# Kernel tuning notes

Measured on AMD Instinct MI355X. Metric: run time of the kernel, lower is better.

## Reference

```python
import jax, jax.numpy as jnp
import numpy as np

N = 4096      # tokens per modality
DIM = 514     # input feature dim
OUT = 256     # out_dim (per-head width, head=1)
NC = 2        # num_classes
LN_EPS = 1e-5


def setup_inputs() -> dict:
    key = jax.random.key(0)
    ks = jax.random.split(key, 12)
    def nrm(k, shape, s=0.02):
        return jax.random.normal(k, shape, dtype=jnp.float32) * s
    return {
        "t1": jax.random.normal(ks[0], (N, DIM), dtype=jnp.float32),
        "t2": jax.random.normal(ks[1], (N, DIM), dtype=jnp.float32),
        "t1c": jax.random.normal(ks[2], (N, DIM), dtype=jnp.float32),
        "Wqkv1": nrm(ks[3], (DIM, 3 * OUT)), "bqkv1": jnp.zeros((3 * OUT,), jnp.float32),
        "Wqkv2": nrm(ks[4], (DIM, 3 * OUT)), "bqkv2": jnp.zeros((3 * OUT,), jnp.float32),
        "Wqkv3": nrm(ks[5], (DIM, 3 * OUT)), "bqkv3": jnp.zeros((3 * OUT,), jnp.float32),
        "Wo1": nrm(ks[6], (2 * OUT, DIM)), "bo1": jnp.zeros((DIM,), jnp.float32),
        "Wo2": nrm(ks[7], (2 * OUT, DIM)), "bo2": jnp.zeros((DIM,), jnp.float32),
        "Wo3": nrm(ks[8], (2 * OUT, DIM)), "bo3": jnp.zeros((DIM,), jnp.float32),
        "ln_g": jnp.ones((3 * DIM,), jnp.float32),
        "ln_b": jnp.zeros((3 * DIM,), jnp.float32),
        "Wh": nrm(ks[9], (3 * DIM, NC)), "bh": jnp.zeros((NC,), jnp.float32),
    }


def _forward(t1, t2, t1c, Wqkv1, bqkv1, Wqkv2, bqkv2, Wqkv3, bqkv3,
             Wo1, bo1, Wo2, bo2, Wo3, bo3, ln_g, ln_b, Wh, bh):
    # QKV projections (head=1 so no head reshape needed)
    q1, k1, v1 = jnp.split(t1 @ Wqkv1 + bqkv1, 3, axis=-1)   # each [n, OUT]
    q2, k2, v2 = jnp.split(t2 @ Wqkv2 + bqkv2, 3, axis=-1)
    q3, k3, v3 = jnp.split(t1c @ Wqkv3 + bqkv3, 3, axis=-1)

    # Six cross-attention instances batched into one group dim g=6.
    # Order: out12, out13, out21, out23, out31, out32  (q_x attends to k_y/v_y)
    qs = jnp.stack([q2, q3, q1, q3, q1, q2])                  # [6, n, OUT]
    ks_ = jnp.stack([k1, k1, k2, k2, k3, k3])
    vs = jnp.stack([v1, v1, v2, v2, v3, v3])
    # NOTE: original code applies NO 1/sqrt(d) scale
    attn = jax.nn.softmax(jnp.einsum('gid,gjd->gij', qs, ks_), axis=-1)
    outs = jnp.einsum('gij,gjd->gid', attn, vs)               # [6, n, OUT]
    out12, out13, out21, out23, out31, out32 = outs

    # residual add with duplicated keys, then per-modality output proj + residual
    t1r = jnp.concatenate([out21, out31], -1) + jnp.concatenate([k1, k1], -1)
    t2r = jnp.concatenate([out12, out32], -1) + jnp.concatenate([k2, k2], -1)
    t3r = jnp.concatenate([out13, out23], -1) + jnp.concatenate([k3, k3], -1)
    a1 = t1r @ Wo1 + bo1 + t1                                 # [n, DIM]
    a2 = t2r @ Wo2 + bo2 + t2
    a3 = t3r @ Wo3 + bo3 + t1c

    atten = jnp.concatenate([a1, a2, a3], -1)                 # [n, 3*DIM]
    mu = jnp.mean(atten, axis=-1, keepdims=True)
    var = jnp.var(atten, axis=-1, keepdims=True)
    normed = (atten - mu) * jax.lax.rsqrt(var + LN_EPS) * ln_g + ln_b
    out = normed @ Wh + bh                                    # [n, NC]
    feat = atten[None]                                        # [1, n, 3*DIM]
    return out, feat


def reference(t1, t2, t1c, Wqkv1, bqkv1, Wqkv2, bqkv2, Wqkv3, bqkv3,
              Wo1, bo1, Wo2, bo2, Wo3, bo3, ln_g, ln_b, Wh, bh):
    return _forward(t1, t2, t1c, Wqkv1, bqkv1, Wqkv2, bqkv2, Wqkv3, bqkv3,
                    Wo1, bo1, Wo2, bo2, Wo3, bo3, ln_g, ln_b, Wh, bh)
```

## Files before the change

### kernel.cpp

```cpp
#include <hip/hip_runtime.h>
#include <hip/hip_bf16.h>

typedef unsigned short u16;
typedef unsigned int u32;
typedef __attribute__((ext_vector_type(8))) __bf16 bf16x8;
typedef __attribute__((ext_vector_type(4))) __bf16 bf16x4;
typedef __attribute__((ext_vector_type(4))) short short4v;
typedef __attribute__((ext_vector_type(4))) float f32x4;
typedef __attribute__((ext_vector_type(16))) float f32x16;

#define N_TOK 4096
#define DIMF  514
#define KPAD  544
#define OUT3  768
#define OUTD  256
#define RDIM  512
#define DIMP  640
#define FDIM  1542
#define SHIFT 16.0f
#define NCHUNK 2
#define KTILES ((N_TOK / NCHUNK) / 16)
#define TILE_U16 8192

__device__ __forceinline__ bf16x8 ld_frag(const u16* p) {
    return __builtin_bit_cast(bf16x8, *reinterpret_cast<const uint4*>(p));
}
__device__ __forceinline__ u16 f2bf(float x) {
    return __builtin_bit_cast(u16, __float2bfloat16(x));
}
__device__ __forceinline__ float bf2f(u16 u) {
    return __bfloat162float(__builtin_bit_cast(__hip_bfloat16, u));
}
__device__ __forceinline__ f32x16 mfma_b(bf16x8 a, bf16x8 b, f32x16 c) {
    return __builtin_amdgcn_mfma_f32_32x32x16_bf16(a, b, c, 0, 0, 0);
}
__device__ __forceinline__ f32x4 mfma16(bf16x8 a, bf16x8 b, f32x4 c) {
    return __builtin_amdgcn_mfma_f32_16x16x32_bf16(a, b, c, 0, 0, 0);
}
__device__ __forceinline__ f32x4 mfma16k16(bf16x4 a, bf16x4 b, f32x4 c) {
#if __has_builtin(__builtin_amdgcn_mfma_f32_16x16x16_bf16)
    return __builtin_amdgcn_mfma_f32_16x16x16_bf16(a, b, c, 0, 0, 0);
#elif __has_builtin(__builtin_amdgcn_mfma_f32_16x16x16bf16_1k)
    return __builtin_amdgcn_mfma_f32_16x16x16bf16_1k(
        __builtin_bit_cast(short4v, a), __builtin_bit_cast(short4v, b), c, 0, 0, 0);
#else
    asm volatile("v_mfma_f32_16x16x16_bf16 %0, %1, %2, %0"
                 : "+v"(c) : "v"(a), "v"(b));
    return c;
#endif
}
__device__ __forceinline__ void gl_lds16(const u16* g, u16* l) {
    __builtin_amdgcn_global_load_lds(
        (const __attribute__((address_space(1))) void*)(g),
        (__attribute__((address_space(3))) void*)(l), 16, 0, 0);
}

__global__ void prep_kernel(const float* __restrict__ t1, const float* __restrict__ t2,
                            const float* __restrict__ t1c,
                            const float* __restrict__ W1, const float* __restrict__ W2,
                            const float* __restrict__ W3,
                            const float* __restrict__ Wo1, const float* __restrict__ Wo2,
                            const float* __restrict__ Wo3,
                            u16* __restrict__ tA, u16* __restrict__ WqkvT,
                            u16* __restrict__ WoT)
{
    int idx = blockIdx.x * blockDim.x + threadIdx.x;
    const int TA_N = 3 * N_TOK * KPAD;
    const int WQ_N = 3 * OUT3 * KPAD;
    const int WO_N = 3 * DIMP * RDIM;
    if (idx < TA_N) {
        int m = idx / (N_TOK * KPAD);
        int rem = idx - m * (N_TOK * KPAD);
        int row = rem / KPAD;
        int col = rem - row * KPAD;
        const float* t = (m == 0) ? t1 : (m == 1) ? t2 : t1c;
        tA[idx] = (col < DIMF) ? f2bf(t[row * DIMF + col]) : (u16)0;
    } else if (idx < TA_N + WQ_N) {
        int i = idx - TA_N;
        int m = i / (OUT3 * KPAD);
        int rem = i - m * (OUT3 * KPAD);
        int n = rem / KPAD;
        int c = rem - n * KPAD;
        const float* W = (m == 0) ? W1 : (m == 1) ? W2 : W3;
        WqkvT[i] = (c < DIMF) ? f2bf(W[c * OUT3 + n]) : (u16)0;
    } else if (idx < TA_N + WQ_N + WO_N) {
        int i = idx - TA_N - WQ_N;
        int m = i / (DIMP * RDIM);
        int rem = i - m * (DIMP * RDIM);
        int n = rem / RDIM;
        int c = rem - n * RDIM;
        const float* W = (m == 0) ? Wo1 : (m == 1) ? Wo2 : Wo3;
        WoT[i] = (n < DIMF) ? f2bf(W[c * DIMF + n]) : (u16)0;
    }
}

__global__ __launch_bounds__(256, 2) void qkv_gemm(
    const u16* __restrict__ tA, const u16* __restrict__ WqkvT,
    const float* __restrict__ b1, const float* __restrict__ b2, const float* __restrict__ b3,
    u16* __restrict__ qbuf, u16* __restrict__ kbuf, u16* __restrict__ vT)
{
    const int mt = blockIdx.x, nt = blockIdx.y, mod = blockIdx.z;
    const u16* A = tA + mod * (N_TOK * KPAD);
    const u16* B = WqkvT + mod * (OUT3 * KPAD);
    const float* bias = (mod == 0) ? b1 : (mod == 1) ? b2 : b3;

    __shared__ alignas(16) u16 Fbuf[2][16 * 512];

    const int tid = threadIdx.x;
    const int lane = tid & 63;
    const int w = tid >> 6;
    const int wm = w & 1, wn = w >> 1;
    const int l31 = lane & 31, h = lane >> 5;

    auto stage = [&](int kt, u16* dst) {
#pragma unroll
        for (int fi = 0; fi < 4; fi++) {
            int f = w * 4 + fi;
            int rb = (f & 7) >> 1, kc = f & 1;
            const u16* src = (f < 8)
                ? &A[(mt * 128 + rb * 32 + l31) * KPAD + kt * 32 + kc * 16 + h * 8]
                : &B[(nt * 128 + rb * 32 + l31) * KPAD + kt * 32 + kc * 16 + h * 8];
            gl_lds16(src, dst + f * 512);
        }
    };

    f32x16 acc[2][2];
#pragma unroll
    for (int i = 0; i < 2; i++)
#pragma unroll
        for (int j = 0; j < 2; j++)
#pragma unroll
            for (int r = 0; r < 16; r++) acc[i][j][r] = 0.f;

    stage(0, Fbuf[0]);
    __syncthreads();

    for (int kt = 0; kt < KPAD / 32; kt++) {
        const int p = kt & 1;
        if (kt + 1 < KPAD / 32) stage(kt + 1, Fbuf[p ^ 1]);
        const u16* FB = Fbuf[p];
#pragma unroll
        for (int kc = 0; kc < 2; kc++) {
            bf16x8 af[2], bfr[2];
#pragma unroll
            for (int mr = 0; mr < 2; mr++)
                af[mr] = ld_frag(&FB[((wm * 2 + mr) * 2 + kc) * 512 + lane * 8]);
#pragma unroll
            for (int nr = 0; nr < 2; nr++)
                bfr[nr] = ld_frag(&FB[(8 + (wn * 2 + nr) * 2 + kc) * 512 + lane * 8]);
#pragma unroll
            for (int mr = 0; mr < 2; mr++)
#pragma unroll
                for (int nr = 0; nr < 2; nr++)
                    acc[mr][nr] = mfma_b(af[mr], bfr[nr], acc[mr][nr]);
        }
        __syncthreads();
    }

    u16* qb = qbuf + mod * (N_TOK * OUTD);
    u16* kb = kbuf + mod * (N_TOK * OUTD);
    u16* vb = vT + mod * (OUTD * N_TOK);
#pragma unroll
    for (int mr = 0; mr < 2; mr++)
#pragma unroll
        for (int nr = 0; nr < 2; nr++)
#pragma unroll
            for (int r = 0; r < 16; r++) {
                int row = mt * 128 + wm * 64 + mr * 32 + (r & 3) + 8 * (r >> 2) + 4 * h;
                int col = nt * 128 + wn * 64 + nr * 32 + l31;
                u16 bv = f2bf(acc[mr][nr][r] + bias[col]);
                int cs = col >> 8, cc = col & 255;
                if (cs == 0)      qb[row * OUTD + cc] = bv;
                else if (cs == 1) kb[row * OUTD + cc] = bv;
                else              vb[cc * N_TOK + row] = bv;
            }
}

__global__ __launch_bounds__(256, 3) void attn_kernel(
    const u16* __restrict__ qbuf, const u16* __restrict__ kbuf,
    const u16* __restrict__ vT, u16* __restrict__ Opart, float* __restrict__ lpart)
{
    const int qt = blockIdx.x;
    const int g  = blockIdx.y;
    const int c  = blockIdx.z;
    const int kv = g >> 1;
    const int mn = (kv == 0) ? 1 : 0;
    const int mx = (kv == 2) ? 1 : 2;
    const int qm = (g & 1) ? mx : mn;

    const u16* Qg = qbuf + qm * (N_TOK * OUTD);
    const u16* Kg = kbuf + kv * (N_TOK * OUTD);
    const u16* Vg = vT + kv * (OUTD * N_TOK);
    u16* Op = Opart + ((size_t)(c * 6 + g) * N_TOK + qt * 64) * OUTD;
    float* lp = lpart + (c * 6 + g) * N_TOK + qt * 64;

    __shared__ alignas(16) u16 Fbuf[2][TILE_U16];

    const int tid = threadIdx.x;
    const int lane = tid & 63;
    const int w = tid >> 6;
    const int sl = lane & 15, sg = lane >> 4;
    const int l31 = lane & 31, h = lane >> 5;
    const int q0 = qt * 64 + w * 16;

    auto stage = [&](int k0, u16* dst) {
        if (w < 2) {
#pragma unroll
            for (int fi = 0; fi < 4; fi++) {
                int j = w * 4 + fi;
                gl_lds16(&Kg[(k0 + sl) * OUTD + j * 32 + sg * 8], dst + j * 512);
            }
        } else {
#pragma unroll
            for (int fi = 0; fi < 4; fi++) {
                int sv = (w - 2) * 4 + fi;
                gl_lds16(&Vg[(sv * 32 + l31) * N_TOK + k0 + h * 8],
                         dst + (8 + sv) * 512);
            }
        }
    };

    const int k0base = c * (N_TOK / NCHUNK);

    stage(k0base, Fbuf[0]);

    bf16x8 qf[8];
#pragma unroll
    for (int j = 0; j < 8; j++)
        qf[j] = ld_frag(&Qg[(q0 + sl) * OUTD + j * 32 + sg * 8]);

    f32x4 Oacc[16];
#pragma unroll
    for (int nb = 0; nb < 16; nb++)
#pragma unroll
        for (int r = 0; r < 4; r++) Oacc[nb][r] = 0.f;
    float lsum = 0.f;

    __syncthreads();

    for (int kt = 0; kt < KTILES; kt++) {
        const int p = kt & 1;
        if (kt + 1 < KTILES) stage(k0base + (kt + 1) * 16, Fbuf[p ^ 1]);
        const u16* FB = Fbuf[p];

        f32x4 Sa, Sb;
#pragma unroll
        for (int r = 0; r < 4; r++) { Sa[r] = 0.f; Sb[r] = 0.f; }
        __builtin_amdgcn_s_setprio(1);
#pragma unroll
        for (int j = 0; j < 4; j++) {
            bf16x8 kfa = ld_frag(&FB[j * 512 + lane * 8]);
            bf16x8 kfb = ld_frag(&FB[(4 + j) * 512 + lane * 8]);
            Sa = mfma16(kfa, qf[j], Sa);
            Sb = mfma16(kfb, qf[4 + j], Sb);
        }
        __builtin_amdgcn_s_setprio(0);

        float e0 = __expf(Sa[0] + Sb[0] - SHIFT);
        float e1 = __expf(Sa[1] + Sb[1] - SHIFT);
        float e2 = __expf(Sa[2] + Sb[2] - SHIFT);
        float e3 = __expf(Sa[3] + Sb[3] - SHIFT);
        lsum += (e0 + e1) + (e2 + e3);
        uint2 pbu;
        pbu.x = (u32)f2bf(e0) | ((u32)f2bf(e1) << 16);
        pbu.y = (u32)f2bf(e2) | ((u32)f2bf(e3) << 16);
        bf16x4 pb = __builtin_bit_cast(bf16x4, pbu);

        __builtin_amdgcn_s_setprio(1);
#pragma unroll
        for (int nb = 0; nb < 16; nb++) {
            int voff = (8 + (nb >> 1)) * 512
                     + ((nb & 1) * 16 + sl + 32 * (sg >> 1)) * 8 + (sg & 1) * 4;
            bf16x4 vf = __builtin_bit_cast(bf16x4,
                *reinterpret_cast<const uint2*>(&FB[voff]));
            Oacc[nb] = mfma16k16(vf, pb, Oacc[nb]);
        }
        __builtin_amdgcn_s_setprio(0);
        __syncthreads();
    }

    lsum += __shfl_xor(lsum, 16, 64);
    lsum += __shfl_xor(lsum, 32, 64);
    if (lane < 16) lp[w * 16 + lane] = lsum;

    float* Tb = reinterpret_cast<float*>(&Fbuf[0][0]) + w * (16 * 17);
#pragma unroll
    for (int nb = 0; nb < 16; nb++) {
#pragma unroll
        for (int r = 0; r < 4; r++)
            Tb[(sg * 4 + r) * 17 + sl] = Oacc[nb][r];
        __builtin_amdgcn_s_waitcnt(0);
        int qq = lane >> 2, d4 = (lane & 3) * 4;
        float v0 = Tb[(d4 + 0) * 17 + qq];
        float v1 = Tb[(d4 + 1) * 17 + qq];
        float v2 = Tb[(d4 + 2) * 17 + qq];
        float v3 = Tb[(d4 + 3) * 17 + qq];
        uint2 sv;
        sv.x = (u32)f2bf(v0) | ((u32)f2bf(v1) << 16);
        sv.y = (u32)f2bf(v2) | ((u32)f2bf(v3) << 16);
        *reinterpret_cast<uint2*>(&Op[(w * 16 + qq) * OUTD + nb * 16 + d4]) = sv;
        __builtin_amdgcn_s_waitcnt(0);
    }
}

__global__ __launch_bounds__(256, 1) void combine_kernel(
    const u16* __restrict__ Opart, const float* __restrict__ lpart,
    const u16* __restrict__ kbuf, u16* __restrict__ rbuf)
{
    const int q = blockIdx.x;
    const int g = blockIdx.y;
    const int d = threadIdx.x;
    const int kv = g >> 1;
    const int mn = (kv == 0) ? 1 : 0;
    const int mx = (kv == 2) ? 1 : 2;
    const int qm = (g & 1) ? mx : mn;
    const int sm = (qm == 0) ? 1 : 0;
    const int slot = (kv == sm) ? 0 : 1;

    float o = 0.f, l = 0.f;
#pragma unroll
    for (int c = 0; c < NCHUNK; c++) {
        o += bf2f(Opart[((size_t)(c * 6 + g) * N_TOK + q) * OUTD + d]);
        l += lpart[(c * 6 + g) * N_TOK + q];
    }
    float res = o / l + bf2f(kbuf[qm * (N_TOK * OUTD) + q * OUTD + d]);
    rbuf[qm * (size_t)(N_TOK * RDIM) + q * RDIM + slot * OUTD + d] = f2bf(res);
}

__global__ __launch_bounds__(256, 2) void proj_gemm(
    const u16* __restrict__ rbuf, const u16* __restrict__ WoT,
    const float* __restrict__ bo1, const float* __restrict__ bo2, const float* __restrict__ bo3,
    const float* __restrict__ t1, const float* __restrict__ t2, const float* __restrict__ t1c,
    float* __restrict__ feat)
{
    const int mt = blockIdx.x, nt = blockIdx.y, mod = blockIdx.z;
    const u16* A = rbuf + mod * (N_TOK * RDIM);
    const u16* B = WoT + mod * (DIMP * RDIM);
    const float* bias = (mod == 0) ? bo1 : (mod == 1) ? bo2 : bo3;
    const float* tres = (mod == 0) ? t1 : (mod == 1) ? t2 : t1c;

    __shared__ alignas(16) u16 Fbuf[2][16 * 512];

    const int tid = threadIdx.x;
    const int lane = tid & 63;
    const int w = tid >> 6;
    const int wm = w & 1, wn = w >> 1;
    const int l31 = lane & 31, h = lane >> 5;

    auto stage = [&](int kt, u16* dst) {
#pragma unroll
        for (int fi = 0; fi < 4; fi++) {
            int f = w * 4 + fi;
            int rb = (f & 7) >> 1, kc = f & 1;
            const u16* src = (f < 8)
                ? &A[(mt * 128 + rb * 32 + l31) * RDIM + kt * 32 + kc * 16 + h * 8]
                : &B[(nt * 128 + rb * 32 + l31) * RDIM + kt * 32 + kc * 16 + h * 8];
            gl_lds16(src, dst + f * 512);
        }
    };

    f32x16 acc[2][2];
#pragma unroll
    for (int i = 0; i < 2; i++)
#pragma unroll
        for (int j = 0; j < 2; j++)
#pragma unroll
            for (int r = 0; r < 16; r++) acc[i][j][r] = 0.f;

    stage(0, Fbuf[0]);
    __syncthreads();

    for (int kt = 0; kt < RDIM / 32; kt++) {
        const int p = kt & 1;
        if (kt + 1 < RDIM / 32) stage(kt + 1, Fbuf[p ^ 1]);
        const u16* FB = Fbuf[p];
#pragma unroll
        for (int kc = 0; kc < 2; kc++) {
            bf16x8 af[2], bfr[2];
#pragma unroll
            for (int mr = 0; mr < 2; mr++)
                af[mr] = ld_frag(&FB[((wm * 2 + mr) * 2 + kc) * 512 + lane * 8]);
#pragma unroll
            for (int nr = 0; nr < 2; nr++)
                bfr[nr] = ld_frag(&FB[(8 + (wn * 2 + nr) * 2 + kc) * 512 + lane * 8]);
#pragma unroll
            for (int mr = 0; mr < 2; mr++)
#pragma unroll
                for (int nr = 0; nr < 2; nr++)
                    acc[mr][nr] = mfma_b(af[mr], bfr[nr], acc[mr][nr]);
        }
        __syncthreads();
    }

#pragma unroll
    for (int mr = 0; mr < 2; mr++)
#pragma unroll
        for (int nr = 0; nr < 2; nr++)
#pragma unroll
            for (int r = 0; r < 16; r++) {
                int row = mt * 128 + wm * 64 + mr * 32 + (r & 3) + 8 * (r >> 2) + 4 * h;
                int col = nt * 128 + wn * 64 + nr * 32 + l31;
                if (col < DIMF) {
                    float v = acc[mr][nr][r] + bias[col] + tres[row * DIMF + col];
                    feat[row * FDIM + mod * DIMF + col] = v;
                }
            }
}

__global__ __launch_bounds__(256, 1) void ln_head(
    const float* __restrict__ feat, const float* __restrict__ gam,
    const float* __restrict__ bet, const float* __restrict__ Wh,
    const float* __restrict__ bh, float* __restrict__ out)
{
    const int row = blockIdx.x;
    const float* x = feat + row * FDIM;
    const int tid = threadIdx.x;
    float v[7];
    float s = 0.f, ss = 0.f;
#pragma unroll
    for (int i = 0; i < 7; i++) {
        int idx = tid + i * 256;
        float val = (idx < FDIM) ? x[idx] : 0.f;
        v[i] = val; s += val; ss += val * val;
    }
#pragma unroll
    for (int m = 1; m < 64; m <<= 1) { s += __shfl_xor(s, m, 64); ss += __shfl_xor(ss, m, 64); }
    __shared__ float red[8];
    const int w = tid >> 6, lane = tid & 63;
    if (lane == 0) { red[w] = s; red[4 + w] = ss; }
    __syncthreads();
    s = red[0] + red[1] + red[2] + red[3];
    ss = red[4] + red[5] + red[6] + red[7];
    const float mu = s / (float)FDIM;
    const float var = ss / (float)FDIM - mu * mu;
    const float rstd = rsqrtf(var + 1e-5f);
    float a0 = 0.f, a1 = 0.f;
#pragma unroll
    for (int i = 0; i < 7; i++) {
        int idx = tid + i * 256;
        if (idx < FDIM) {
            float nv = (v[i] - mu) * rstd * gam[idx] + bet[idx];
            a0 += nv * Wh[idx * 2];
            a1 += nv * Wh[idx * 2 + 1];
        }
    }
#pragma unroll
    for (int m = 1; m < 64; m <<= 1) { a0 += __shfl_xor(a0, m, 64); a1 += __shfl_xor(a1, m, 64); }
    __shared__ float red2[8];
    if (lane == 0) { red2[w] = a0; red2[4 + w] = a1; }
    __syncthreads();
    if (tid == 0) {
        out[row * 2 + 0] = red2[0] + red2[1] + red2[2] + red2[3] + bh[0];
        out[row * 2 + 1] = red2[4] + red2[5] + red2[6] + red2[7] + bh[1];
    }
}

extern "C" void kernel_launch(void* const* d_in, const int* in_sizes, int n_in,
                              void* d_out, int out_size, void* d_ws, size_t ws_size,
                              hipStream_t stream)
{
    const float* t1    = (const float*)d_in[0];
    const float* t2    = (const float*)d_in[1];
    const float* t1c   = (const float*)d_in[2];
    const float* Wqkv1 = (const float*)d_in[3];
    const float* bqkv1 = (const float*)d_in[4];
    const float* Wqkv2 = (const float*)d_in[5];
    const float* bqkv2 = (const float*)d_in[6];
    const float* Wqkv3 = (const float*)d_in[7];
    const float* bqkv3 = (const float*)d_in[8];
    const float* Wo1   = (const float*)d_in[9];
    const float* bo1   = (const float*)d_in[10];
    const float* Wo2   = (const float*)d_in[11];
    const float* bo2   = (const float*)d_in[12];
    const float* Wo3   = (const float*)d_in[13];
    const float* bo3   = (const float*)d_in[14];
    const float* ln_g  = (const float*)d_in[15];
    const float* ln_b  = (const float*)d_in[16];
    const float* Wh    = (const float*)d_in[17];
    const float* bh    = (const float*)d_in[18];

    char* ws = (char*)d_ws;
    size_t off = 0;
    u16* tA    = (u16*)(ws + off); off += (size_t)3 * N_TOK * KPAD * 2;
    u16* WqkvT = (u16*)(ws + off); off += (size_t)3 * OUT3 * KPAD * 2;
    u16* WoT   = (u16*)(ws + off); off += (size_t)3 * DIMP * RDIM * 2;
    u16* qbuf  = (u16*)(ws + off); off += (size_t)3 * N_TOK * OUTD * 2;
    u16* kbuf  = (u16*)(ws + off); off += (size_t)3 * N_TOK * OUTD * 2;
    u16* vT    = (u16*)(ws + off); off += (size_t)3 * OUTD * N_TOK * 2;
    u16* rbuf  = (u16*)(ws + off); off += (size_t)3 * N_TOK * RDIM * 2;
    u16* Opart = (u16*)(ws + off); off += (size_t)NCHUNK * 6 * N_TOK * OUTD * 2;
    float* lpart = (float*)(ws + off); off += (size_t)NCHUNK * 6 * N_TOK * 4;

    float* out  = (float*)d_out;
    float* feat = out + N_TOK * 2;

    const int prep_total = 3 * N_TOK * KPAD + 3 * OUT3 * KPAD + 3 * DIMP * RDIM;
    prep_kernel<<<(prep_total + 255) / 256, 256, 0, stream>>>(
        t1, t2, t1c, Wqkv1, Wqkv2, Wqkv3, Wo1, Wo2, Wo3, tA, WqkvT, WoT);

    qkv_gemm<<<dim3(32, 6, 3), 256, 0, stream>>>(
        tA, WqkvT, bqkv1, bqkv2, bqkv3, qbuf, kbuf, vT);

    attn_kernel<<<dim3(64, 6, NCHUNK), 256, 0, stream>>>(qbuf, kbuf, vT, Opart, lpart);

    combine_kernel<<<dim3(N_TOK, 6), 256, 0, stream>>>(Opart, lpart, kbuf, rbuf);

    proj_gemm<<<dim3(32, 5, 3), 256, 0, stream>>>(
        rbuf, WoT, bo1, bo2, bo3, t1, t2, t1c, feat);

    ln_head<<<4096, 256, 0, stream>>>(feat, ln_g, ln_b, Wh, bh, out);
}
```

Before: 402.8 us.

## Use 32-key tiles with K=32 MFMA for PV and split K/V staging

Doubles the key tile to 32 per iteration so the P·V product can use the 16x16x32 bf16 MFMA instead of 16x16x16, halving the PV MFMA count per key. K is double-buffered and prefetched one tile ahead, while V is staged single-buffered within each iteration. Explicit vmcnt waits and raw barriers replace __syncthreads. The row permutation in K staging makes the QK output layout line up with the PV B-operand. This exposes the V load latency within each iteration and depends on hand-counted vmcnt values being correct.

```diff
diff --git a/kernel.cpp b/kernel.cpp
--- a/kernel.cpp
+++ b/kernel.cpp
@@ -4,8 +4,6 @@
 typedef unsigned short u16;
 typedef unsigned int u32;
 typedef __attribute__((ext_vector_type(8))) __bf16 bf16x8;
-typedef __attribute__((ext_vector_type(4))) __bf16 bf16x4;
-typedef __attribute__((ext_vector_type(4))) short short4v;
 typedef __attribute__((ext_vector_type(4))) float f32x4;
 typedef __attribute__((ext_vector_type(16))) float f32x16;
 
@@ -19,8 +17,7 @@
 #define FDIM  1542
 #define SHIFT 16.0f
 #define NCHUNK 2
-#define KTILES ((N_TOK / NCHUNK) / 16)
-#define TILE_U16 8192
+#define KTILES ((N_TOK / NCHUNK) / 32)
 
 __device__ __forceinline__ bf16x8 ld_frag(const u16* p) {
     return __builtin_bit_cast(bf16x8, *reinterpret_cast<const uint4*>(p));
@@ -36,18 +33,6 @@
 }
 __device__ __forceinline__ f32x4 mfma16(bf16x8 a, bf16x8 b, f32x4 c) {
     return __builtin_amdgcn_mfma_f32_16x16x32_bf16(a, b, c, 0, 0, 0);
-}
-__device__ __forceinline__ f32x4 mfma16k16(bf16x4 a, bf16x4 b, f32x4 c) {
-#if __has_builtin(__builtin_amdgcn_mfma_f32_16x16x16_bf16)
-    return __builtin_amdgcn_mfma_f32_16x16x16_bf16(a, b, c, 0, 0, 0);
-#elif __has_builtin(__builtin_amdgcn_mfma_f32_16x16x16bf16_1k)
-    return __builtin_amdgcn_mfma_f32_16x16x16bf16_1k(
-        __builtin_bit_cast(short4v, a), __builtin_bit_cast(short4v, b), c, 0, 0, 0);
-#else
-    asm volatile("v_mfma_f32_16x16x16_bf16 %0, %1, %2, %0"
-                 : "+v"(c) : "v"(a), "v"(b));
-    return c;
-#endif
 }
 __device__ __forceinline__ void gl_lds16(const u16* g, u16* l) {
     __builtin_amdgcn_global_load_lds(
@@ -194,35 +179,37 @@
     u16* Op = Opart + ((size_t)(c * 6 + g) * N_TOK + qt * 64) * OUTD;
     float* lp = lpart + (c * 6 + g) * N_TOK + qt * 64;
 
-    __shared__ alignas(16) u16 Fbuf[2][TILE_U16];
+    __shared__ alignas(16) u16 Kb[2][16 * 512];
+    __shared__ alignas(16) u16 Vb[16 * 512];
 
     const int tid = threadIdx.x;
     const int lane = tid & 63;
     const int w = tid >> 6;
     const int sl = lane & 15, sg = lane >> 4;
-    const int l31 = lane & 31, h = lane >> 5;
     const int q0 = qt * 64 + w * 16;
-
-    auto stage = [&](int k0, u16* dst) {
-        if (w < 2) {
-#pragma unroll
-            for (int fi = 0; fi < 4; fi++) {
-                int j = w * 4 + fi;
-                gl_lds16(&Kg[(k0 + sl) * OUTD + j * 32 + sg * 8], dst + j * 512);
-            }
-        } else {
-#pragma unroll
-            for (int fi = 0; fi < 4; fi++) {
-                int sv = (w - 2) * 4 + fi;
-                gl_lds16(&Vg[(sv * 32 + l31) * N_TOK + k0 + h * 8],
-                         dst + (8 + sv) * 512);
-            }
+    const int krow = (sl >> 2) * 8 + (sl & 3);
+
+    auto stageK = [&](int k0, u16* dst) {
+#pragma unroll
+        for (int fi = 0; fi < 4; fi++) {
+            int f = w * 4 + fi;
+            int cc = f >> 3, j = f & 7;
+            gl_lds16(&Kg[(k0 + krow + cc * 4) * OUTD + j * 32 + sg * 8],
+                     dst + f * 512);
         }
     };
+    auto stageV = [&](int k0) {
+#pragma unroll
+        for (int fi = 0; fi < 4; fi++) {
+            int nb = w * 4 + fi;
+            gl_lds16(&Vg[(size_t)(nb * 16 + sl) * N_TOK + k0 + sg * 8],
+                     Vb + nb * 512);
+        }
+    };
 
     const int k0base = c * (N_TOK / NCHUNK);
 
-    stage(k0base, Fbuf[0]);
+    stageK(k0base, Kb[0]);
 
     bf16x8 qf[8];
 #pragma unroll
@@ -236,54 +223,66 @@
         for (int r = 0; r < 4; r++) Oacc[nb][r] = 0.f;
     float lsum = 0.f;
 
-    __syncthreads();
-
     for (int kt = 0; kt < KTILES; kt++) {
         const int p = kt & 1;
-        if (kt + 1 < KTILES) stage(k0base + (kt + 1) * 16, Fbuf[p ^ 1]);
-        const u16* FB = Fbuf[p];
-
-        f32x4 Sa, Sb;
-#pragma unroll
-        for (int r = 0; r < 4; r++) { Sa[r] = 0.f; Sb[r] = 0.f; }
+        const int k0 = k0base + kt * 32;
+
+        stageV(k0);
+        if (kt + 1 < KTILES) {
+            stageK(k0 + 32, Kb[p ^ 1]);
+            asm volatile("s_waitcnt vmcnt(8)" ::: "memory");
+        } else {
+            asm volatile("s_waitcnt vmcnt(4)" ::: "memory");
+        }
+        __builtin_amdgcn_s_barrier();
+
+        const u16* KB = Kb[p];
+        f32x4 S0, S1;
+#pragma unroll
+        for (int r = 0; r < 4; r++) { S0[r] = 0.f; S1[r] = 0.f; }
         __builtin_amdgcn_s_setprio(1);
 #pragma unroll
-        for (int j = 0; j < 4; j++) {
-            bf16x8 kfa = ld_frag(&FB[j * 512 + lane * 8]);
-            bf16x8 kfb = ld_frag(&FB[(4 + j) * 512 + lane * 8]);
-            Sa = mfma16(kfa, qf[j], Sa);
-            Sb = mfma16(kfb, qf[4 + j], Sb);
+        for (int j = 0; j < 8; j++) {
+            bf16x8 kf0 = ld_frag(&KB[j * 512 + lane * 8]);
+            bf16x8 kf1 = ld_frag(&KB[(8 + j) * 512 + lane * 8]);
+            S0 = mfma16(kf0, qf[j], S0);
+            S1 = mfma16(kf1, qf[j], S1);
         }
         __builtin_amdgcn_s_setprio(0);
 
-        float e0 = __expf(Sa[0] + Sb[0] - SHIFT);
-        float e1 = __expf(Sa[1] + Sb[1] - SHIFT);
-        float e2 = __expf(Sa[2] + Sb[2] - SHIFT);
-        float e3 = __expf(Sa[3] + Sb[3] - SHIFT);
-        lsum += (e0 + e1) + (e2 + e3);
-        uint2 pbu;
-        pbu.x = (u32)f2bf(e0) | ((u32)f2bf(e1) << 16);
-        pbu.y = (u32)f2bf(e2) | ((u32)f2bf(e3) << 16);
-        bf16x4 pb = __builtin_bit_cast(bf16x4, pbu);
+        float e0 = __expf(S0[0] - SHIFT), e1 = __expf(S0[1] - SHIFT);
+        float e2 = __expf(S0[2] - SHIFT), e3 = __expf(S0[3] - SHIFT);
+        float e4 = __expf(S1[0] - SHIFT), e5 = __expf(S1[1] - SHIFT);
+        float e6 = __expf(S1[2] - SHIFT), e7 = __expf(S1[3] - SHIFT);
+        lsum += ((e0 + e1) + (e2 + e3)) + ((e4 + e5) + (e6 + e7));
+        uint4 bu;
+        bu.x = (u32)f2bf(e0) | ((u32)f2bf(e1) << 16);
+        bu.y = (u32)f2bf(e2) | ((u32)f2bf(e3) << 16);
+        bu.z = (u32)f2bf(e4) | ((u32)f2bf(e5) << 16);
+        bu.w = (u32)f2bf(e6) | ((u32)f2bf(e7) << 16);
+        bf16x8 pb = __builtin_bit_cast(bf16x8, bu);
+
+        if (kt + 1 < KTILES)
+            asm volatile("s_waitcnt vmcnt(4)" ::: "memory");
+        else
+            asm volatile("s_waitcnt vmcnt(0)" ::: "memory");
+        __builtin_amdgcn_s_barrier();
 
         __builtin_amdgcn_s_setprio(1);
 #pragma unroll
         for (int nb = 0; nb < 16; nb++) {
-            int voff = (8 + (nb >> 1)) * 512
-                     + ((nb & 1) * 16 + sl + 32 * (sg >> 1)) * 8 + (sg & 1) * 4;
-            bf16x4 vf = __builtin_bit_cast(bf16x4,
-                *reinterpret_cast<const uint2*>(&FB[voff]));
-            Oacc[nb] = mfma16k16(vf, pb, Oacc[nb]);
+            bf16x8 vf = ld_frag(&Vb[nb * 512 + lane * 8]);
+            Oacc[nb] = mfma16(vf, pb, Oacc[nb]);
         }
         __builtin_amdgcn_s_setprio(0);
-        __syncthreads();
+        __builtin_amdgcn_s_barrier();
     }
 
     lsum += __shfl_xor(lsum, 16, 64);
     lsum += __shfl_xor(lsum, 32, 64);
     if (lane < 16) lp[w * 16 + lane] = lsum;
 
-    float* Tb = reinterpret_cast<float*>(&Fbuf[0][0]) + w * (16 * 17);
+    float* Tb = reinterpret_cast<float*>(&Vb[0]) + w * (16 * 17);
 #pragma unroll
     for (int nb = 0; nb < 16; nb++) {
 #pragma unroll
```

Measured after the change: 416.0 us. 3.3% more time.
